# Kernel tuning notes

Measured on AMD Instinct MI355X. Metric: run time of the kernel, lower is better.

Reference implementation:

```python
import jax, jax.numpy as jnp
import numpy as np

B, S, E, H, DK, DV, V, FH = 2, 1024, 1024, 16, 64, 64, 32000, 512


def _posenc(seq_len, d_model, n=10000.0):
    pos = jnp.arange(seq_len, dtype=jnp.float32)[:, None]            # [S,1]
    i2 = jnp.arange(0, d_model, 2, dtype=jnp.float32)                 # [E/2]
    ang = pos / jnp.power(n, i2 / d_model)                            # [S,E/2]
    return jnp.stack([jnp.sin(ang), jnp.cos(ang)], axis=-1).reshape(seq_len, d_model)


def _norm(x, g, b, eps=1e-15):
    m = jnp.mean(x, axis=-1, keepdims=True)
    v = jnp.var(x, axis=-1, keepdims=True)  # unbiased=False
    return g * (x - m) * jax.lax.rsqrt(v + eps) + b


def _ff(x, w1, b1, w2, b2):
    return jax.nn.relu(x @ w1 + b1) @ w2 + b2


def _mha(xq, xkv, wqkv, bqkv, wo, bo, causal):
    # wqkv: [3,H,E,d], bqkv: [3,H,d]  (stacked per-head linears)
    q = jnp.einsum('bse,hek->bhsk', xq, wqkv[0]) + bqkv[0][None, :, None, :]
    k = jnp.einsum('bse,hek->bhsk', xkv, wqkv[1]) + bqkv[1][None, :, None, :]
    v = jnp.einsum('bse,hev->bhsv', xkv, wqkv[2]) + bqkv[2][None, :, None, :]
    s = jnp.einsum('bhqk,bhsk->bhqs', q, k) / jnp.sqrt(jnp.float32(DK))
    if causal:
        mask = jnp.triu(jnp.ones((S, S), dtype=bool), 1)
        s = jnp.where(mask[None, None], -jnp.inf, s)
    p = jax.nn.softmax(s, axis=-1)
    o = jnp.einsum('bhqs,bhsv->bhqv', p, v)
    o = o.transpose(0, 2, 1, 3).reshape(xq.shape[0], S, H * DV)
    return o @ wo + bo


def setup_inputs():
    key = jax.random.key(0)
    ks = iter(jax.random.split(key, 40))

    def rn(shape, scale=0.02):
        return jax.random.normal(next(ks), shape, dtype=jnp.float32) * scale

    inp = {
        'src': jax.random.randint(next(ks), (B, S), 0, V, dtype=jnp.int32),
        'trg': jax.random.randint(next(ks), (B, S), 0, V, dtype=jnp.int32),
        'emb_enc': rn((V, E), 1.0),
        'emb_dec': rn((V, E), 1.0),
        'qkv_e': rn((3, H, E, DK)), 'bqkv_e': rn((3, H, DK)),
        'wo_e': rn((H * DV, E)), 'bo_e': rn((E,)),
        'qkv_m': rn((3, H, E, DK)), 'bqkv_m': rn((3, H, DK)),
        'wo_m': rn((H * DV, E)), 'bo_m': rn((E,)),
        'qkv_c': rn((3, H, E, DK)), 'bqkv_c': rn((3, H, DK)),
        'wo_c': rn((H * DV, E)), 'bo_c': rn((E,)),
        'gamma': jnp.ones((5, E), jnp.float32),
        'beta': jnp.zeros((5, E), jnp.float32),
        'ff_w1': rn((2, E, FH)), 'ff_b1': rn((2, FH)),
        'ff_w2': rn((2, FH, E)), 'ff_b2': rn((2, E)),
        'w_out': rn((E, V)), 'b_out': rn((V,)),
    }
    return inp


def reference(src, trg, emb_enc, emb_dec, qkv_e, bqkv_e, wo_e, bo_e,
              qkv_m, bqkv_m, wo_m, bo_m, qkv_c, bqkv_c, wo_c, bo_c,
              gamma, beta, ff_w1, ff_b1, ff_w2, ff_b2, w_out, b_out):
    pe = _posenc(S, E)
    # ---- encoder ----
    x = emb_enc[src] + pe
    a = _mha(x, x, qkv_e, bqkv_e, wo_e, bo_e, causal=False)
    n1 = _norm(x + a, gamma[0], beta[0])
    f = _ff(n1, ff_w1[0], ff_b1[0], ff_w2[0], ff_b2[0])
    enc = _norm(n1 + f, gamma[1], beta[1])
    # ---- decoder ----
    y = emb_dec[trg] + pe
    a = _mha(y, y, qkv_m, bqkv_m, wo_m, bo_m, causal=True)
    n1d = _norm(y + a, gamma[2], beta[2])
    a2 = _mha(n1d, enc, qkv_c, bqkv_c, wo_c, bo_c, causal=False)
    n2d = _norm(n1d + a2, gamma[3], beta[3])
    f = _ff(n2d, ff_w1[1], ff_b1[1], ff_w2[1], ff_b2[1])
    n3d = _norm(n2d + f, gamma[4], beta[4])
    logits = n3d @ w_out + b_out
    return jax.nn.softmax(logits, axis=-1)
```

## Files before the change

kernel.cpp:

```cpp
#include <hip/hip_runtime.h>
#include <hip/hip_bf16.h>
#include <hip/hip_fp16.h>
#include <math.h>

namespace {

constexpr int kB = 2, kS = 1024, kE = 1024, kH = 16, kD = 64, kV = 32000, kFH = 512;
constexpr int kBS = kB * kS;
constexpr int kHD = kH * kD;

typedef __attribute__((ext_vector_type(8))) short bf16x8;
typedef __attribute__((ext_vector_type(8))) unsigned short u16x8;
typedef __attribute__((ext_vector_type(4))) float f32x4;

#define GLDS(g, l) __builtin_amdgcn_global_load_lds(                          \
      (const __attribute__((address_space(1))) void*)(g),                     \
      (__attribute__((address_space(3))) void*)(l), 16, 0, 0)

__global__ __launch_bounds__(256) void pe_table_k(float* __restrict__ pe) {
  int s = blockIdx.x;
  float* dst = pe + (size_t)s * kE;
  for (int e = threadIdx.x; e < kE; e += 256) {
    int i = e >> 1;
    float denom = powf(10000.0f, (float)(2 * i) * (1.0f / (float)kE));
    float ang = (float)s / denom;
    dst[e] = (e & 1) ? cosf(ang) : sinf(ang);
  }
}

__global__ __launch_bounds__(256) void embed_pe_k(const int* __restrict__ tok,
                                                  const float* __restrict__ emb,
                                                  const float* __restrict__ pe,
                                                  float* __restrict__ out,
                                                  __hip_bfloat16* __restrict__ outb) {
  int row = blockIdx.x;
  int s = row & (kS - 1);
  int t = tok[row];
  const float4* src = (const float4*)(emb + (size_t)t * kE);
  const float4* per = (const float4*)(pe + (size_t)s * kE);
  float4* dst = (float4*)(out + (size_t)row * kE);
  __hip_bfloat16* dstb = outb + (size_t)row * kE;
  for (int e4 = threadIdx.x; e4 < kE / 4; e4 += 256) {
    float4 a = src[e4], p = per[e4];
    float4 v = make_float4(a.x + p.x, a.y + p.y, a.z + p.z, a.w + p.w);
    dst[e4] = v;
    union { __hip_bfloat16 h[4]; short4 s4; } u;
    u.h[0] = __float2bfloat16(v.x); u.h[1] = __float2bfloat16(v.y);
    u.h[2] = __float2bfloat16(v.z); u.h[3] = __float2bfloat16(v.w);
    ((short4*)dstb)[e4] = u.s4;
  }
}

struct TSeg {
  const float* src;
  __hip_bfloat16* dst;
  int R, C, bpi, off;
};
struct TcastArgs { TSeg s[11]; };

__global__ __launch_bounds__(256) void tcast_all_k(TcastArgs a) {
  __shared__ float tile[32][33];
  int bid = blockIdx.x;
  int si = 0;
#pragma unroll
  for (int i = 1; i < 11; ++i) si = (bid >= a.s[i].off) ? i : si;
  const TSeg sg = a.s[si];
  int local = bid - sg.off;
  int item = local / sg.bpi;
  int rem  = local % sg.bpi;
  int nbx = sg.C >> 5;
  int c0 = (rem % nbx) * 32, r0 = (rem / nbx) * 32;
  const float* src = sg.src + (size_t)item * sg.R * sg.C;
  __hip_bfloat16* dst = sg.dst + (size_t)item * sg.R * sg.C;
  int tx = threadIdx.x & 31, ty = threadIdx.x >> 5;
#pragma unroll
  for (int i = 0; i < 32; i += 8)
    tile[ty + i][tx] = src[(size_t)(r0 + ty + i) * sg.C + c0 + tx];
  __syncthreads();
#pragma unroll
  for (int i = 0; i < 32; i += 8)
    dst[(size_t)(c0 + ty + i) * sg.R + r0 + tx] = __float2bfloat16(tile[tx][ty + i]);
}

__global__ __launch_bounds__(256) void vtrans_k(const __hip_bfloat16* __restrict__ v,
                                                int sV, __hip_bfloat16* __restrict__ vt) {
  __shared__ unsigned short tile[32][34];
  int s0 = blockIdx.x * 32, d0 = blockIdx.y * 32, bh = blockIdx.z;
  int b = bh >> 4, h = bh & 15;
  int tx = threadIdx.x & 31, ty = threadIdx.x >> 5;
  const unsigned short* src = (const unsigned short*)v;
  unsigned short* dst = (unsigned short*)vt;
#pragma unroll
  for (int i = 0; i < 32; i += 8)
    tile[ty + i][tx] = src[(size_t)(b * kS + s0 + ty + i) * sV + h * 64 + d0 + tx];
  __syncthreads();
#pragma unroll
  for (int i = 0; i < 32; i += 8)
    dst[(size_t)(bh * 64 + d0 + ty + i) * kS + s0 + tx] = tile[tx][ty + i];
}

__global__ __launch_bounds__(256) void gemm_bf16_k(
    const __hip_bfloat16* __restrict__ A,
    const __hip_bfloat16* __restrict__ Bt,
    const float* __restrict__ bias,
    void* __restrict__ Cout,
    int N, int K, int mode, int gridM) {
  __shared__ __align__(16) char L[3][16384];
  const int nwg = gridDim.x, id = blockIdx.x;
  const int swz = (id & 7) * (nwg >> 3) + (id >> 3);
  const int bm = (swz % gridM) * 128, bn = (swz / gridM) * 128;
  const int tid = threadIdx.x, w = tid >> 6, lane = tid & 63;
  const int wr = w >> 1, wc = w & 1;
  const int lr = lane & 15, kg = lane >> 4;
  const int NT = K >> 5;
  const __hip_bfloat16* Ag = A + (size_t)bm * K;
  const __hip_bfloat16* Bg = Bt + (size_t)bn * K;

  auto stage = [&](int t) {
    const int buf = t % 3, k0 = t * 32;
#pragma unroll
    for (int j = 0; j < 2; ++j) {
      int slot = w * 64 + lane + j * 256;
      int row = slot >> 2;
      int cs = (slot & 3) ^ ((row >> 1) & 3);
      GLDS(Ag + (size_t)row * K + k0 + cs * 8, L[buf] + w * 1024 + j * 4096);
      GLDS(Bg + (size_t)row * K + k0 + cs * 8, L[buf] + 8192 + w * 1024 + j * 4096);
    }
  };

  f32x4 acc[4][4] = {};
  stage(0);
  stage(1);
  asm volatile("s_waitcnt vmcnt(4)" ::: "memory");
  __builtin_amdgcn_s_barrier();

  for (int t = 0; t < NT; ++t) {
    const char* buf = L[t % 3];
    if (t + 2 < NT) stage(t + 2);
    bf16x8 af[4], bfr[4];
#pragma unroll
    for (int i = 0; i < 4; ++i) {
      int row = wr * 64 + i * 16 + lr;
      af[i] = *(const bf16x8*)(buf + row * 64 + ((kg ^ ((row >> 1) & 3)) << 4));
    }
#pragma unroll
    for (int j = 0; j < 4; ++j) {
      int row = wc * 64 + j * 16 + lr;
      bfr[j] = *(const bf16x8*)(buf + 8192 + row * 64 + ((kg ^ ((row >> 1) & 3)) << 4));
    }
    __builtin_amdgcn_s_setprio(1);
#pragma unroll
    for (int i = 0; i < 4; ++i)
#pragma unroll
      for (int j = 0; j < 4; ++j)
        acc[i][j] = __builtin_amdgcn_mfma_f32_16x16x32_bf16(af[i], bfr[j], acc[i][j], 0, 0, 0);
    __builtin_amdgcn_s_setprio(0);
    if (t + 2 < NT)
      asm volatile("s_waitcnt vmcnt(4) lgkmcnt(0)" ::: "memory");
    else
      asm volatile("s_waitcnt vmcnt(0) lgkmcnt(0)" ::: "memory");
    __builtin_amdgcn_s_barrier();
  }

  float* Cf = (float*)Cout;
  __hip_bfloat16* Cb = (__hip_bfloat16*)Cout;
#pragma unroll
  for (int j = 0; j < 4; ++j) {
    int col = bn + wc * 64 + j * 16 + lr;
    float bc = bias[col];
#pragma unroll
    for (int i = 0; i < 4; ++i) {
      int rbase = bm + wr * 64 + i * 16 + kg * 4;
#pragma unroll
      for (int r = 0; r < 4; ++r) {
        float val = acc[i][j][r] + bc;
        if (mode & 1) val = fmaxf(val, 0.0f);
        if (mode < 2) Cf[(size_t)(rbase + r) * N + col] = val;
        else          Cb[(size_t)(rbase + r) * N + col] = __float2bfloat16(val);
      }
    }
  }
}

__global__ __launch_bounds__(512, 2) void gemm256_k(
    const __hip_bfloat16* __restrict__ A,
    const __hip_bfloat16* __restrict__ Bt,
    const float* __restrict__ bias,
    __half* __restrict__ C,
    int N, int K, int gridM) {
  __shared__ __align__(16) char L[3][32768];
  const int tid = threadIdx.x, w = tid >> 6, lane = tid & 63;
  const int wm = w >> 2, wn = w & 3;
  const int lr = lane & 15, kg = lane >> 4;
  const int nwg = gridDim.x, id = blockIdx.x;
  const int swz = (id & 7) * (nwg >> 3) + (id >> 3);
  const int bm = (swz % gridM) * 256, bn = (swz / gridM) * 256;
  const int NT = K >> 5;
  const __hip_bfloat16* Ag = A + (size_t)bm * K;
  const __hip_bfloat16* Bg = Bt + (size_t)bn * K;

  auto stage = [&](int t) {
    const int buf = t % 3, k0 = t * 32;
#pragma unroll
    for (int j = 0; j < 2; ++j) {
      int slot = w * 64 + lane + j * 512;
      int row = slot >> 2;
      int cs = (slot & 3) ^ ((row >> 1) & 3);
      GLDS(Ag + (size_t)row * K + k0 + cs * 8, L[buf] + w * 1024 + j * 8192);
      GLDS(Bg + (size_t)row * K + k0 + cs * 8, L[buf] + 16384 + w * 1024 + j * 8192);
    }
  };

  f32x4 acc[8][4] = {};
  stage(0);
  stage(1);
  asm volatile("s_waitcnt vmcnt(4)" ::: "memory");
  __builtin_amdgcn_s_barrier();

  for (int t = 0; t < NT; ++t) {
    const char* buf = L[t % 3];
    if (t + 2 < NT) stage(t + 2);
    bf16x8 af[8], bfr[4];
#pragma unroll
    for (int mg = 0; mg < 8; ++mg) {
      int row = wm * 128 + mg * 16 + lr;
      af[mg] = *(const bf16x8*)(buf + row * 64 + ((kg ^ ((row >> 1) & 3)) << 4));
    }
#pragma unroll
    for (int n = 0; n < 4; ++n) {
      int row = wn * 64 + n * 16 + lr;
      bfr[n] = *(const bf16x8*)(buf + 16384 + row * 64 + ((kg ^ ((row >> 1) & 3)) << 4));
    }
    __builtin_amdgcn_s_setprio(1);
#pragma unroll
    for (int mg = 0; mg < 8; ++mg)
#pragma unroll
      for (int n = 0; n < 4; ++n)
        acc[mg][n] = __builtin_amdgcn_mfma_f32_16x16x32_bf16(af[mg], bfr[n], acc[mg][n], 0, 0, 0);
    __builtin_amdgcn_s_setprio(0);
    if (t + 2 < NT)
      asm volatile("s_waitcnt vmcnt(4) lgkmcnt(0)" ::: "memory");
    else
      asm volatile("s_waitcnt vmcnt(0) lgkmcnt(0)" ::: "memory");
    __builtin_amdgcn_s_barrier();
  }

#pragma unroll
  for (int mg = 0; mg < 8; ++mg) {
    int rbase = bm + wm * 128 + mg * 16 + (kg << 2);
#pragma unroll
    for (int n = 0; n < 4; ++n) {
      int col = bn + (wn << 6) + n * 16 + lr;
      float bc = bias[col];
#pragma unroll
      for (int r = 0; r < 4; ++r)
        C[(size_t)(rbase + r) * N + col] = __float2half(acc[mg][n][r] + bc);
    }
  }
}

__global__ __launch_bounds__(256) void attn_mfma_k(
    const __hip_bfloat16* __restrict__ q, int sQ,
    const __hip_bfloat16* __restrict__ k, int sK,
    const __hip_bfloat16* __restrict__ vt,
    __hip_bfloat16* __restrict__ o,
    int causal) {
  __shared__ __align__(16) char Ks[3][8192];
  __shared__ __align__(16) char Vs[3][8192];
  __shared__ __align__(16) char Ps[4][2304];
  const int tid = threadIdx.x, w = tid >> 6, l = tid & 63;
  const int lr = l & 15, lg = l >> 4;
  const int q0 = blockIdx.x * 64, h = blockIdx.y, b = blockIdx.z;

  const int qrow = q0 + w * 16 + lr;
  const __hip_bfloat16* qp = q + (size_t)(b * kS + qrow) * sQ + h * 64 + lg * 8;
  bf16x8 aQ0 = *(const bf16x8*)qp;
  bf16x8 aQ1 = *(const bf16x8*)(qp + 32);

  f32x4 oacc[4] = {};
  float mrun[4], lrun[4];
#pragma unroll
  for (int r = 0; r < 4; ++r) { mrun[r] = -INFINITY; lrun[r] = 0.0f; }

  const int ntiles = causal ? ((q0 >> 6) + 1) : (kS >> 6);
  const int diagT = causal ? (q0 >> 6) : -1;
  const char* kbase = (const char*)(k + (size_t)(b * kS) * sK + h * 64);
  const char* vbase = (const char*)(vt + (size_t)((b * kH + h) * 64) * kS);
  char* Pw = Ps[w];

  auto stage = [&](int t) {
    const int buf = t % 3, kv0 = t * 64;
#pragma unroll
    for (int i = 0; i < 2; ++i) {
      int slot = w * 128 + i * 64 + l;
      int row = slot >> 3, sl = slot & 7, c = sl ^ (row & 7);
      GLDS(kbase + (size_t)(kv0 + row) * sK * 2 + c * 16, Ks[buf] + (w * 128 + i * 64) * 16);
      GLDS(vbase + (size_t)row * kS * 2 + kv0 * 2 + c * 16, Vs[buf] + (w * 128 + i * 64) * 16);
    }
  };

  stage(0);
  if (ntiles > 1) {
    stage(1);
    asm volatile("s_waitcnt vmcnt(4)" ::: "memory");
  } else {
    asm volatile("s_waitcnt vmcnt(0)" ::: "memory");
  }
  __builtin_amdgcn_s_barrier();

  for (int t = 0; t < ntiles; ++t) {
    const int kv0 = t * 64;
    const char* Kb = Ks[t % 3];
    const char* Vb = Vs[t % 3];
    if (t + 2 < ntiles) stage(t + 2);

    f32x4 sacc[4] = {};
#pragma unroll
    for (int nf = 0; nf < 4; ++nf) {
      int key = nf * 16 + lr;
#pragma unroll
      for (int kf = 0; kf < 2; ++kf) {
        int ch = (lg + kf * 4) ^ (key & 7);
        bf16x8 bK = *(const bf16x8*)(Kb + key * 128 + ch * 16);
        sacc[nf] = __builtin_amdgcn_mfma_f32_16x16x32_bf16(kf ? aQ1 : aQ0, bK, sacc[nf], 0, 0, 0);
      }
    }

#pragma unroll
    for (int r = 0; r < 4; ++r) {
      int row16 = lg * 4 + r;
      int qg = q0 + w * 16 + row16;
      float sv[4];
#pragma unroll
      for (int nf = 0; nf < 4; ++nf) {
        float s = sacc[nf][r] * 0.125f;
        if (t == diagT && (kv0 + nf * 16 + lr) > qg) s = -INFINITY;
        sv[nf] = s;
      }
      float mx = fmaxf(fmaxf(sv[0], sv[1]), fmaxf(sv[2], sv[3]));
#pragma unroll
      for (int m = 1; m < 16; m <<= 1) mx = fmaxf(mx, __shfl_xor(mx, m));
      float mnew = fmaxf(mrun[r], mx);
      float sc = __expf(mrun[r] - mnew);
      mrun[r] = mnew;
      float rs = 0.0f;
#pragma unroll
      for (int nf = 0; nf < 4; ++nf) {
        float p = __expf(sv[nf] - mnew);
        rs += p;
        *(__hip_bfloat16*)(Pw + row16 * 144 + (nf * 16 + lr) * 2) = __float2bfloat16(p);
      }
#pragma unroll
      for (int m = 1; m < 16; m <<= 1) rs += __shfl_xor(rs, m);
      lrun[r] = lrun[r] * sc + rs;
#pragma unroll
      for (int nfd = 0; nfd < 4; ++nfd) oacc[nfd][r] *= sc;
    }

    bf16x8 aP0 = *(const bf16x8*)(Pw + lr * 144 + (lg * 8) * 2);
    bf16x8 aP1 = *(const bf16x8*)(Pw + lr * 144 + (lg * 8 + 32) * 2);
#pragma unroll
    for (int nfd = 0; nfd < 4; ++nfd) {
      int d = nfd * 16 + lr;
#pragma unroll
      for (int kf = 0; kf < 2; ++kf) {
        int ch = (lg + kf * 4) ^ (d & 7);
        bf16x8 bV = *(const bf16x8*)(Vb + d * 128 + ch * 16);
        oacc[nfd] = __builtin_amdgcn_mfma_f32_16x16x32_bf16(kf ? aP1 : aP0, bV, oacc[nfd], 0, 0, 0);
      }
    }

    if (t + 1 < ntiles) {
      if (t + 2 < ntiles)
        asm volatile("s_waitcnt vmcnt(4) lgkmcnt(0)" ::: "memory");
      else
        asm volatile("s_waitcnt vmcnt(0) lgkmcnt(0)" ::: "memory");
      __builtin_amdgcn_s_barrier();
    }
  }

#pragma unroll
  for (int r = 0; r < 4; ++r) {
    float inv = 1.0f / lrun[r];
    int rowg = q0 + w * 16 + lg * 4 + r;
#pragma unroll
    for (int nfd = 0; nfd < 4; ++nfd)
      o[(size_t)(b * kS + rowg) * kHD + h * 64 + nfd * 16 + lr] =
          __float2bfloat16(oacc[nfd][r] * inv);
  }
}

__global__ __launch_bounds__(256) void ln_res_k(const float* __restrict__ a,
                                                const float* __restrict__ b,
                                                const float* __restrict__ gamma,
                                                const float* __restrict__ beta,
                                                float* __restrict__ out,
                                                __hip_bfloat16* __restrict__ outb) {
  __shared__ float sh[10];
  int row = blockIdx.x, tid = threadIdx.x;
  const float4* a4 = (const float4*)(a + (size_t)row * kE);
  const float4* b4 = (const float4*)(b + (size_t)row * kE);
  float4 t = a4[tid], u = b4[tid];
  t.x += u.x; t.y += u.y; t.z += u.z; t.w += u.w;
  float s = t.x + t.y + t.z + t.w;
  float q2 = t.x * t.x + t.y * t.y + t.z * t.z + t.w * t.w;
  for (int o = 32; o > 0; o >>= 1) { s += __shfl_down(s, o); q2 += __shfl_down(q2, o); }
  int lane = tid & 63, wid = tid >> 6;
  if (lane == 0) { sh[wid] = s; sh[4 + wid] = q2; }
  __syncthreads();
  if (tid == 0) {
    float S2 = sh[0] + sh[1] + sh[2] + sh[3];
    float Q2 = sh[4] + sh[5] + sh[6] + sh[7];
    float mean = S2 * (1.0f / kE);
    float var = Q2 * (1.0f / kE) - mean * mean;
    sh[8] = mean;
    sh[9] = rsqrtf(var + 1e-15f);
  }
  __syncthreads();
  float mean = sh[8], inv = sh[9];
  float4 g = ((const float4*)gamma)[tid], be = ((const float4*)beta)[tid];
  float4 v;
  v.x = g.x * ((t.x - mean) * inv) + be.x;
  v.y = g.y * ((t.y - mean) * inv) + be.y;
  v.z = g.z * ((t.z - mean) * inv) + be.z;
  v.w = g.w * ((t.w - mean) * inv) + be.w;
  ((float4*)(out + (size_t)row * kE))[tid] = v;
  union { __hip_bfloat16 h[4]; short4 s4; } uo;
  uo.h[0] = __float2bfloat16(v.x); uo.h[1] = __float2bfloat16(v.y);
  uo.h[2] = __float2bfloat16(v.z); uo.h[3] = __float2bfloat16(v.w);
  ((short4*)(outb + (size_t)row * kE))[tid] = uo.s4;
}

__global__ __launch_bounds__(512) void softmax_rows_k(const __half* __restrict__ lgt,
                                                      float* __restrict__ out) {
  __shared__ float sh[18];
  int row = blockIdx.x;
  const u16x8* x8 = (const u16x8*)(lgt + (size_t)row * kV);
  const int n8 = kV / 8;
  int tid = threadIdx.x;
  u16x8 v[8];
  float m = -INFINITY, sum = 0.0f;
#pragma unroll
  for (int i = 0; i < 8; ++i) {
    int idx = tid + i * 512;
    if (idx < n8) {
      v[i] = x8[idx];
      union { u16x8 u; __half h[8]; } cv; cv.u = v[i];
      float f[8];
#pragma unroll
      for (int j = 0; j < 8; ++j) f[j] = __half2float(cv.h[j]);
      float mx = f[0];
#pragma unroll
      for (int j = 1; j < 8; ++j) mx = fmaxf(mx, f[j]);
      float nm = fmaxf(m, mx);
      float add = 0.0f;
#pragma unroll
      for (int j = 0; j < 8; ++j) add += __expf(f[j] - nm);
      sum = sum * __expf(m - nm) + add;
      m = nm;
    }
  }
  for (int o = 32; o > 0; o >>= 1) {
    float om = __shfl_down(m, o), os = __shfl_down(sum, o);
    float nm = fmaxf(m, om);
    sum = sum * __expf(m - nm) + os * __expf(om - nm);
    m = nm;
  }
  int lane = tid & 63, wid = tid >> 6;
  if (lane == 0) { sh[wid] = m; sh[8 + wid] = sum; }
  __syncthreads();
  if (tid == 0) {
    float M = sh[0], S2 = 0.0f;
#pragma unroll
    for (int i2 = 1; i2 < 8; ++i2) M = fmaxf(M, sh[i2]);
#pragma unroll
    for (int i2 = 0; i2 < 8; ++i2) S2 += sh[8 + i2] * __expf(sh[i2] - M);
    sh[16] = M;
    sh[17] = 1.0f / S2;
  }
  __syncthreads();
  float M = sh[16], rcp = sh[17];
#pragma unroll
  for (int i = 0; i < 8; ++i) {
    int idx = tid + i * 512;
    if (idx < n8) {
      union { u16x8 u; __half h[8]; } cv; cv.u = v[i];
      float4 o0, o1;
      o0.x = __expf(__half2float(cv.h[0]) - M) * rcp;
      o0.y = __expf(__half2float(cv.h[1]) - M) * rcp;
      o0.z = __expf(__half2float(cv.h[2]) - M) * rcp;
      o0.w = __expf(__half2float(cv.h[3]) - M) * rcp;
      o1.x = __expf(__half2float(cv.h[4]) - M) * rcp;
      o1.y = __expf(__half2float(cv.h[5]) - M) * rcp;
      o1.z = __expf(__half2float(cv.h[6]) - M) * rcp;
      o1.w = __expf(__half2float(cv.h[7]) - M) * rcp;
      float* dst = out + (size_t)row * kV + idx * 8;
      ((float4*)dst)[0] = o0;
      ((float4*)dst)[1] = o1;
    }
  }
}

}

extern "C" void kernel_launch(void* const* d_in, const int* in_sizes, int n_in,
                              void* d_out, int out_size, void* d_ws, size_t ws_size,
                              hipStream_t stream) {
  const int*   src    = (const int*)d_in[0];
  const int*   trg    = (const int*)d_in[1];
  const float* emb_e  = (const float*)d_in[2];
  const float* emb_d  = (const float*)d_in[3];
  const float* qkv_e  = (const float*)d_in[4];
  const float* bqkv_e = (const float*)d_in[5];
  const float* wo_e   = (const float*)d_in[6];
  const float* bo_e   = (const float*)d_in[7];
  const float* qkv_m  = (const float*)d_in[8];
  const float* bqkv_m = (const float*)d_in[9];
  const float* wo_m   = (const float*)d_in[10];
  const float* bo_m   = (const float*)d_in[11];
  const float* qkv_c  = (const float*)d_in[12];
  const float* bqkv_c = (const float*)d_in[13];
  const float* wo_c   = (const float*)d_in[14];
  const float* bo_c   = (const float*)d_in[15];
  const float* gamma  = (const float*)d_in[16];
  const float* beta   = (const float*)d_in[17];
  const float* ffw1   = (const float*)d_in[18];
  const float* ffb1   = (const float*)d_in[19];
  const float* ffw2   = (const float*)d_in[20];
  const float* ffb2   = (const float*)d_in[21];
  const float* wout   = (const float*)d_in[22];
  const float* bout   = (const float*)d_in[23];
  float* out = (float*)d_out;

  char* base = (char*)d_ws;
  const size_t R = (size_t)kBS * kE;
  const size_t WE = (size_t)kHD * kE;
  float* enc_x = (float*)base;
  float* dec_x = enc_x + R;
  float* t1    = dec_x + R;
  float* n1    = t1 + R;
  float* n_enc = n1 + R;
  __hip_bfloat16* bb     = (__hip_bfloat16*)(n_enc + R);
  __hip_bfloat16* enc_xb = bb;
  __hip_bfloat16* n1b    = enc_xb + R;
  __hip_bfloat16* n_encb = n1b + R;
  __hip_bfloat16* qkvb   = n_encb + R;
  __hip_bfloat16* kvb    = qkvb + 3 * R;
  __hip_bfloat16* qb1    = kvb + 2 * R;
  __hip_bfloat16* vtb    = qb1 + R;
  __hip_bfloat16* ao16   = vtb + R;
  __hip_bfloat16* ffhb   = ao16 + R;
  __hip_bfloat16* Wqkv_e = ffhb + R / 2;
  __hip_bfloat16* Wqkv_m = Wqkv_e + 3 * WE;
  __hip_bfloat16* Wqkv_c = Wqkv_m + 3 * WE;
  __hip_bfloat16* Wo_e   = Wqkv_c + 3 * WE;
  __hip_bfloat16* Wo_m   = Wo_e + WE;
  __hip_bfloat16* Wo_c   = Wo_m + WE;
  __hip_bfloat16* Wf1a   = Wo_c + WE;
  __hip_bfloat16* Wf1b   = Wf1a + (size_t)kE * kFH;
  __hip_bfloat16* Wf2a   = Wf1b + (size_t)kE * kFH;
  __hip_bfloat16* Wf2b   = Wf2a + (size_t)kFH * kE;
  float* pe = (float*)(Wf2b + (size_t)kFH * kE);
  const size_t lgtBytes = (size_t)kBS * kV * sizeof(__half);
  __hip_bfloat16* dec_xb = (__hip_bfloat16*)(base + lgtBytes);
  __hip_bfloat16* Wv     = dec_xb + R;
  __half* lgt = (__half*)base;

  auto gemmb = [&](const __hip_bfloat16* A, const __hip_bfloat16* Bt, const float* bias,
                   void* C, int M, int N, int K, int mode) {
    int gridM = M / 128;
    gemm_bf16_k<<<dim3(gridM * (N / 128)), 256, 0, stream>>>(A, Bt, bias, C, N, K, mode, gridM);
  };
  auto vtrans = [&](const __hip_bfloat16* v, int sV) {
    vtrans_k<<<dim3(kS / 32, kD / 32, kB * kH), 256, 0, stream>>>(v, sV, vtb);
  };
  auto attn = [&](const __hip_bfloat16* q, int sQ, const __hip_bfloat16* k, int sK,
                  int causal) {
    attn_mfma_k<<<dim3(kS / 64, kH, kB), 256, 0, stream>>>(q, sQ, k, sK, vtb, ao16, causal);
  };
  auto ln = [&](const float* a, const float* b2, int sel, float* o1, __hip_bfloat16* o2) {
    ln_res_k<<<kBS, 256, 0, stream>>>(a, b2, gamma + sel * kE, beta + sel * kE, o1, o2);
  };

  pe_table_k<<<kS, 256, 0, stream>>>(pe);
  {
    TcastArgs a;
    const size_t EF = (size_t)kE * kFH;
    a.s[0]  = {qkv_e,       Wqkv_e, kE, kD,   64,    0};
    a.s[1]  = {qkv_m,       Wqkv_m, kE, kD,   64,    3072};
    a.s[2]  = {qkv_c,       Wqkv_c, kE, kD,   64,    6144};
    a.s[3]  = {wo_e,        Wo_e,   kHD, kE,  1024,  9216};
    a.s[4]  = {wo_m,        Wo_m,   kHD, kE,  1024,  10240};
    a.s[5]  = {wo_c,        Wo_c,   kHD, kE,  1024,  11264};
    a.s[6]  = {ffw1,        Wf1a,   kE, kFH,  512,   12288};
    a.s[7]  = {ffw1 + EF,   Wf1b,   kE, kFH,  512,   12800};
    a.s[8]  = {ffw2,        Wf2a,   kFH, kE,  512,   13312};
    a.s[9]  = {ffw2 + EF,   Wf2b,   kFH, kE,  512,   13824};
    a.s[10] = {wout,        Wv,     kE, kV,   32000, 14336};
    tcast_all_k<<<46336, 256, 0, stream>>>(a);
  }

  embed_pe_k<<<kBS, 256, 0, stream>>>(src, emb_e, pe, enc_x, enc_xb);
  gemmb(enc_xb, Wqkv_e, bqkv_e, qkvb, kBS, 3 * kHD, kE, 2);
  vtrans(qkvb + 2 * kHD, 3 * kHD);
  attn(qkvb, 3 * kHD, qkvb + kHD, 3 * kHD, 0);
  gemmb(ao16, Wo_e, bo_e, t1, kBS, kE, kHD, 0);
  ln(enc_x, t1, 0, n1, n1b);
  gemmb(n1b, Wf1a, ffb1, ffhb, kBS, kFH, kE, 3);
  gemmb(ffhb, Wf2a, ffb2, t1, kBS, kE, kFH, 0);
  ln(n1, t1, 1, n_enc, n_encb);

  embed_pe_k<<<kBS, 256, 0, stream>>>(trg, emb_d, pe, dec_x, dec_xb);
  gemmb(dec_xb, Wqkv_m, bqkv_m, qkvb, kBS, 3 * kHD, kE, 2);
  vtrans(qkvb + 2 * kHD, 3 * kHD);
  attn(qkvb, 3 * kHD, qkvb + kHD, 3 * kHD, 1);
  gemmb(ao16, Wo_m, bo_m, t1, kBS, kE, kHD, 0);
  ln(dec_x, t1, 2, n1, n1b);

  gemmb(n1b, Wqkv_c, bqkv_c, qb1, kBS, kHD, kE, 2);
  gemmb(n_encb, Wqkv_c + WE, bqkv_c + kHD, kvb, kBS, 2 * kHD, kE, 2);
  vtrans(kvb + kHD, 2 * kHD);
  attn(qb1, kHD, kvb, 2 * kHD, 0);
  gemmb(ao16, Wo_c, bo_c, t1, kBS, kE, kHD, 0);
  ln(n1, t1, 3, enc_x, enc_xb);

  gemmb(enc_xb, Wf1b, ffb1 + kFH, ffhb, kBS, kFH, kE, 3);
  gemmb(ffhb, Wf2b, ffb2 + kE, t1, kBS, kE, kFH, 0);
  ln(enc_x, t1, 4, dec_x, dec_xb);

  gemm256_k<<<dim3((kBS / 256) * (kV / 256)), 512, 0, stream>>>(
      dec_xb, Wv, bout, lgt, kV, kE, kBS / 256);
  softmax_rows_k<<<kBS, 512, 0, stream>>>(lgt, out);
}
```

Before: 660.3 us.

## Fuse embedding, positional encoding and weight cast into one prep kernel; lazy softmax rescale

```diff
diff --git a/kernel.cpp b/kernel.cpp
--- a/kernel.cpp
+++ b/kernel.cpp
@@ -16,40 +16,6 @@
 #define GLDS(g, l) __builtin_amdgcn_global_load_lds(                          \
       (const __attribute__((address_space(1))) void*)(g),                     \
       (__attribute__((address_space(3))) void*)(l), 16, 0, 0)
-
-__global__ __launch_bounds__(256) void pe_table_k(float* __restrict__ pe) {
-  int s = blockIdx.x;
-  float* dst = pe + (size_t)s * kE;
-  for (int e = threadIdx.x; e < kE; e += 256) {
-    int i = e >> 1;
-    float denom = powf(10000.0f, (float)(2 * i) * (1.0f / (float)kE));
-    float ang = (float)s / denom;
-    dst[e] = (e & 1) ? cosf(ang) : sinf(ang);
-  }
-}
-
-__global__ __launch_bounds__(256) void embed_pe_k(const int* __restrict__ tok,
-                                                  const float* __restrict__ emb,
-                                                  const float* __restrict__ pe,
-                                                  float* __restrict__ out,
-                                                  __hip_bfloat16* __restrict__ outb) {
-  int row = blockIdx.x;
-  int s = row & (kS - 1);
-  int t = tok[row];
-  const float4* src = (const float4*)(emb + (size_t)t * kE);
-  const float4* per = (const float4*)(pe + (size_t)s * kE);
-  float4* dst = (float4*)(out + (size_t)row * kE);
-  __hip_bfloat16* dstb = outb + (size_t)row * kE;
-  for (int e4 = threadIdx.x; e4 < kE / 4; e4 += 256) {
-    float4 a = src[e4], p = per[e4];
-    float4 v = make_float4(a.x + p.x, a.y + p.y, a.z + p.z, a.w + p.w);
-    dst[e4] = v;
-    union { __hip_bfloat16 h[4]; short4 s4; } u;
-    u.h[0] = __float2bfloat16(v.x); u.h[1] = __float2bfloat16(v.y);
-    u.h[2] = __float2bfloat16(v.z); u.h[3] = __float2bfloat16(v.w);
-    ((short4*)dstb)[e4] = u.s4;
-  }
-}
 
 struct TSeg {
   const float* src;
@@ -58,9 +24,40 @@
 };
 struct TcastArgs { TSeg s[11]; };
 
-__global__ __launch_bounds__(256) void tcast_all_k(TcastArgs a) {
+__global__ __launch_bounds__(256) void prep_k(
+    const int* __restrict__ src, const int* __restrict__ trg,
+    const float* __restrict__ emb_e, const float* __restrict__ emb_d,
+    float* __restrict__ enc_x, __hip_bfloat16* __restrict__ enc_xb,
+    float* __restrict__ dec_x, __hip_bfloat16* __restrict__ dec_xb,
+    TcastArgs a) {
+  int bid = blockIdx.x;
+  if (bid < 2 * kBS) {
+    int which = bid >> 11;
+    int row = bid & (kBS - 1);
+    const int* tok = which ? trg : src;
+    const float* emb = which ? emb_d : emb_e;
+    float* out = which ? dec_x : enc_x;
+    __hip_bfloat16* outb = which ? dec_xb : enc_xb;
+    int s = row & (kS - 1);
+    int t = tok[row];
+    const float4* sv4 = (const float4*)(emb + (size_t)t * kE);
+    int e4 = threadIdx.x;
+    float4 aa = sv4[e4];
+    const float kLn = 0.017988946039015984f;
+    int p0 = e4 * 2, p1 = p0 + 1;
+    float a0 = (float)s * __expf(-(float)p0 * kLn);
+    float a1 = (float)s * __expf(-(float)p1 * kLn);
+    float4 v = make_float4(aa.x + sinf(a0), aa.y + cosf(a0),
+                           aa.z + sinf(a1), aa.w + cosf(a1));
+    ((float4*)(out + (size_t)row * kE))[e4] = v;
+    union { __hip_bfloat16 h[4]; short4 s4; } u;
+    u.h[0] = __float2bfloat16(v.x); u.h[1] = __float2bfloat16(v.y);
+    u.h[2] = __float2bfloat16(v.z); u.h[3] = __float2bfloat16(v.w);
+    ((short4*)(outb + (size_t)row * kE))[e4] = u.s4;
+    return;
+  }
+  bid -= 2 * kBS;
   __shared__ float tile[32][33];
-  int bid = blockIdx.x;
   int si = 0;
 #pragma unroll
   for (int i = 1; i < 11; ++i) si = (bid >= a.s[i].off) ? i : si;
@@ -70,16 +67,16 @@
   int rem  = local % sg.bpi;
   int nbx = sg.C >> 5;
   int c0 = (rem % nbx) * 32, r0 = (rem / nbx) * 32;
-  const float* src = sg.src + (size_t)item * sg.R * sg.C;
-  __hip_bfloat16* dst = sg.dst + (size_t)item * sg.R * sg.C;
+  const float* srcp = sg.src + (size_t)item * sg.R * sg.C;
+  __hip_bfloat16* dstp = sg.dst + (size_t)item * sg.R * sg.C;
   int tx = threadIdx.x & 31, ty = threadIdx.x >> 5;
 #pragma unroll
   for (int i = 0; i < 32; i += 8)
-    tile[ty + i][tx] = src[(size_t)(r0 + ty + i) * sg.C + c0 + tx];
+    tile[ty + i][tx] = srcp[(size_t)(r0 + ty + i) * sg.C + c0 + tx];
   __syncthreads();
 #pragma unroll
   for (int i = 0; i < 32; i += 8)
-    dst[(size_t)(c0 + ty + i) * sg.R + r0 + tx] = __float2bfloat16(tile[tx][ty + i]);
+    dstp[(size_t)(c0 + ty + i) * sg.R + r0 + tx] = __float2bfloat16(tile[tx][ty + i]);
 }
 
 __global__ __launch_bounds__(256) void vtrans_k(const __hip_bfloat16* __restrict__ v,
@@ -340,21 +337,24 @@
       float mx = fmaxf(fmaxf(sv[0], sv[1]), fmaxf(sv[2], sv[3]));
 #pragma unroll
       for (int m = 1; m < 16; m <<= 1) mx = fmaxf(mx, __shfl_xor(mx, m));
-      float mnew = fmaxf(mrun[r], mx);
-      float sc = __expf(mrun[r] - mnew);
-      mrun[r] = mnew;
+      if (mx > mrun[r] + 8.0f) {
+        float sc = __expf(mrun[r] - mx);
+        mrun[r] = mx;
+        lrun[r] *= sc;
+#pragma unroll
+        for (int nfd = 0; nfd < 4; ++nfd) oacc[nfd][r] *= sc;
+      }
+      float base = mrun[r];
       float rs = 0.0f;
 #pragma unroll
       for (int nf = 0; nf < 4; ++nf) {
-        float p = __expf(sv[nf] - mnew);
+        float p = __expf(sv[nf] - base);
         rs += p;
         *(__hip_bfloat16*)(Pw + row16 * 144 + (nf * 16 + lr) * 2) = __float2bfloat16(p);
       }
 #pragma unroll
       for (int m = 1; m < 16; m <<= 1) rs += __shfl_xor(rs, m);
-      lrun[r] = lrun[r] * sc + rs;
-#pragma unroll
-      for (int nfd = 0; nfd < 4; ++nfd) oacc[nfd][r] *= sc;
+      lrun[r] += rs;
     }
 
     bf16x8 aP0 = *(const bf16x8*)(Pw + lr * 144 + (lg * 8) * 2);
@@ -560,7 +560,6 @@
   __hip_bfloat16* Wf1b   = Wf1a + (size_t)kE * kFH;
   __hip_bfloat16* Wf2a   = Wf1b + (size_t)kE * kFH;
   __hip_bfloat16* Wf2b   = Wf2a + (size_t)kFH * kE;
-  float* pe = (float*)(Wf2b + (size_t)kFH * kE);
   const size_t lgtBytes = (size_t)kBS * kV * sizeof(__half);
   __hip_bfloat16* dec_xb = (__hip_bfloat16*)(base + lgtBytes);
   __hip_bfloat16* Wv     = dec_xb + R;
@@ -582,7 +581,6 @@
     ln_res_k<<<kBS, 256, 0, stream>>>(a, b2, gamma + sel * kE, beta + sel * kE, o1, o2);
   };
 
-  pe_table_k<<<kS, 256, 0, stream>>>(pe);
   {
     TcastArgs a;
     const size_t EF = (size_t)kE * kFH;
@@ -597,10 +595,10 @@
     a.s[8]  = {ffw2,        Wf2a,   kFH, kE,  512,   13312};
     a.s[9]  = {ffw2 + EF,   Wf2b,   kFH, kE,  512,   13824};
     a.s[10] = {wout,        Wv,     kE, kV,   32000, 14336};
-    tcast_all_k<<<46336, 256, 0, stream>>>(a);
-  }
-
-  embed_pe_k<<<kBS, 256, 0, stream>>>(src, emb_e, pe, enc_x, enc_xb);
+    prep_k<<<2 * kBS + 46336, 256, 0, stream>>>(src, trg, emb_e, emb_d,
+                                                enc_x, enc_xb, dec_x, dec_xb, a);
+  }
+
   gemmb(enc_xb, Wqkv_e, bqkv_e, qkvb, kBS, 3 * kHD, kE, 2);
   vtrans(qkvb + 2 * kHD, 3 * kHD);
   attn(qkvb, 3 * kHD, qkvb + kHD, 3 * kHD, 0);
@@ -610,7 +608,6 @@
   gemmb(ffhb, Wf2a, ffb2, t1, kBS, kE, kFH, 0);
   ln(n1, t1, 1, n_enc, n_encb);
 
-  embed_pe_k<<<kBS, 256, 0, stream>>>(trg, emb_d, pe, dec_x, dec_xb);
   gemmb(dec_xb, Wqkv_m, bqkv_m, qkvb, kBS, 3 * kHD, kE, 2);
   vtrans(qkvb + 2 * kHD, 3 * kHD);
   attn(qkvb, 3 * kHD, qkvb + kHD, 3 * kHD, 1);
```

Result: no change. 648.2 us (-1.8%).
